# Kernel tuning notes

Hardware: AMD Instinct MI355X
Metric: run time of the kernel (lower is better)

## Reference

```python
import jax, jax.numpy as jnp
import numpy as np

D_MODEL = 512
N_HEADS = 8
D_KEYS = D_MODEL // N_HEADS  # 64
DIN = D_MODEL * 2            # 1024
DPROJ = D_KEYS * N_HEADS * 2 # 1024
B, L = 2, 2048


def setup_inputs() -> dict:
    key = jax.random.key(0)
    ks = jax.random.split(key, 11)
    s_in = 1.0 / np.sqrt(DIN)
    s_out = 1.0 / np.sqrt(DPROJ)
    return {
        "queries": jax.random.normal(ks[0], (B, L, DIN), jnp.float32),
        "keys": jax.random.normal(ks[1], (B, L, DIN), jnp.float32),
        "values": jax.random.normal(ks[2], (B, L, DIN), jnp.float32),
        "Wq": jax.random.normal(ks[3], (DPROJ, DIN), jnp.float32) * s_in,
        "bq": jax.random.normal(ks[4], (DPROJ,), jnp.float32) * s_in,
        "Wk": jax.random.normal(ks[5], (DPROJ, DIN), jnp.float32) * s_in,
        "bk": jax.random.normal(ks[6], (DPROJ,), jnp.float32) * s_in,
        "Wv": jax.random.normal(ks[7], (DPROJ, DIN), jnp.float32) * s_in,
        "bv": jax.random.normal(ks[8], (DPROJ,), jnp.float32) * s_in,
        "Wo": jax.random.normal(ks[9], (DIN, DPROJ), jnp.float32) * s_out,
        "bo": jax.random.normal(ks[10], (DIN,), jnp.float32) * s_out,
    }


def reference(queries, keys, values, Wq, bq, Wk, bk, Wv, bv, Wo, bo):
    b, l, _ = queries.shape
    H, E = N_HEADS, 2
    # projections: (B, L, DIN) -> (B, L, d_keys, H, 2)
    q = (queries @ Wq.T + bq).reshape(b, l, -1, H, E)
    k = (keys @ Wk.T + bk).reshape(b, l, -1, H, E)
    v = (values @ Wv.T + bv).reshape(b, l, -1, H, E)
    scale = 1.0 / np.sqrt(E)  # E=2 (real/imag)
    # attention over the d_keys axis, per token n, per head h
    scores = jnp.einsum('bnlhe,bnshe->bnhls', q, k)  # (B, L, H, dk, dk)
    A = jax.nn.softmax(scale * scores, axis=-1)
    out = jnp.einsum('bnhls,bnshd->bnlhd', A, v)     # (B, L, dk, H, 2)
    out = out.reshape(b, l, -1)                      # (B, L, dk*H*2)
    return out @ Wo.T + bo                           # (B, L, 2*d_model)
```

## Files before the change

### kernel.cpp

```cpp
#include <hip/hip_runtime.h>
#include <hip/hip_bf16.h>
#include <stdint.h>

#define TOK   4096
#define KDIM  1024
#define NDIM  1024
#define NHEAD 8

typedef _Float16 f16;
typedef __attribute__((ext_vector_type(8))) _Float16 f16x8;
typedef __attribute__((ext_vector_type(4))) float f32x4;

__device__ __forceinline__ void gload_lds16(const void* g, void* l) {
    __builtin_amdgcn_global_load_lds(
        (const __attribute__((address_space(1))) void*)g,
        (__attribute__((address_space(3))) void*)l, 16, 0, 0);
}

struct CvtArgs {
    const float* src[7];
    f16*         dst[7];
    int          n4[7];
};

__global__ __launch_bounds__(256) void cvt_kernel(CvtArgs a) {
    const int seg = blockIdx.y;
    const float4* s = (const float4*)a.src[seg];
    f16* d = a.dst[seg];
    const int n4 = a.n4[seg];
    const int stride = gridDim.x * blockDim.x;
    for (int i = blockIdx.x * blockDim.x + threadIdx.x; i < n4; i += stride) {
        float4 v = s[i];
        union { f16 h[4]; uint2 u; } o;
        o.h[0] = (f16)v.x; o.h[1] = (f16)v.y; o.h[2] = (f16)v.z; o.h[3] = (f16)v.w;
        *(uint2*)(d + (size_t)i * 4) = o.u;
    }
}

struct GemmArgs {
    const f16*   A[3];
    const f16*   B[3];
    const float* bias[3];
    void*        C[3];
};

#define VM_WAIT6 asm volatile("s_waitcnt vmcnt(6)" ::: "memory")
#define VM_WAIT0 asm volatile("s_waitcnt vmcnt(0)" ::: "memory")

template<int OUTMODE>
__global__ __launch_bounds__(256) void gemm_bt_kernel(GemmArgs ga) {
    constexpr int K = KDIM, N = NDIM;
    constexpr int NT = K / 64;
    const f16*   A    = ga.A[blockIdx.z];
    const f16*   B    = ga.B[blockIdx.z];
    const float* bias = ga.bias[blockIdx.z];

    __shared__ f16 sm[2 * (128 * 64 + 64 * 64)];

    const int tid  = threadIdx.x;
    const int wave = tid >> 6, lane = tid & 63;
    const int wm = wave >> 1, wn = wave & 1;
    const int bm = blockIdx.x * 128, bn = blockIdx.y * 64;
    const int lrow = lane & 15, kgrp = lane >> 4;

    f32x4 acc[4][2] = {};

    const int colL = (lane & 7) << 3;
    const int colG = (((lane & 7) ^ ((lane >> 3) & 7)) << 3);
    const int arow = wave * 32 + (lane >> 3);
    const int brow = wave * 16 + (lane >> 3);

    auto stage = [&](int buf, int kt) {
        f16* As = sm + buf * (128 * 64 + 64 * 64);
        f16* Bs = As + 128 * 64;
        #pragma unroll
        for (int i = 0; i < 4; ++i) {
            const int row = arow + i * 8;
            gload_lds16(A + (size_t)(bm + row) * K + kt + colG, As + row * 64 + colL);
        }
        #pragma unroll
        for (int i = 0; i < 2; ++i) {
            const int row = brow + i * 8;
            gload_lds16(B + (size_t)(bn + row) * K + kt + colG, Bs + row * 64 + colL);
        }
    };

    stage(0, 0);

    const int swz = (lrow & 7) << 3;

    for (int it = 0; it < NT; ++it) {
        const int cur = it & 1;
        if (it + 1 < NT) {
            stage(cur ^ 1, (it + 1) * 64);
            VM_WAIT6;
        } else {
            VM_WAIT0;
        }
        __builtin_amdgcn_s_barrier();
        __builtin_amdgcn_sched_barrier(0);

        const f16* As = sm + cur * (128 * 64 + 64 * 64);
        const f16* Bs = As + 128 * 64;
        #pragma unroll
        for (int kk = 0; kk < 2; ++kk) {
            f16x8 af[4], bf[2];
            const int kcol = (kk * 32 + kgrp * 8) ^ swz;
            #pragma unroll
            for (int mi = 0; mi < 4; ++mi)
                af[mi] = *(const f16x8*)(As + (wm * 64 + mi * 16 + lrow) * 64 + kcol);
            #pragma unroll
            for (int ni = 0; ni < 2; ++ni)
                bf[ni] = *(const f16x8*)(Bs + (wn * 32 + ni * 16 + lrow) * 64 + kcol);
            #pragma unroll
            for (int mi = 0; mi < 4; ++mi)
                #pragma unroll
                for (int ni = 0; ni < 2; ++ni)
                    acc[mi][ni] = __builtin_amdgcn_mfma_f32_16x16x32_f16(af[mi], bf[ni], acc[mi][ni], 0, 0, 0);
        }
        __builtin_amdgcn_s_barrier();
    }

    const int rbase = kgrp * 4;
    #pragma unroll
    for (int mi = 0; mi < 4; ++mi) {
        #pragma unroll
        for (int ni = 0; ni < 2; ++ni) {
            const int col = bn + wn * 32 + ni * 16 + lrow;
            const float bv = bias[col];
            #pragma unroll
            for (int r = 0; r < 4; ++r) {
                const int row = bm + wm * 64 + mi * 16 + rbase + r;
                const float v = acc[mi][ni][r] + bv;
                if constexpr (OUTMODE == 0)
                    ((f16*)ga.C[blockIdx.z])[(size_t)row * N + col] = (f16)v;
                else
                    ((float*)ga.C[blockIdx.z])[(size_t)row * N + col] = v;
            }
        }
    }
}

__global__ __launch_bounds__(512) void attn_kernel(const f16* qp, const f16* kp,
                                                   const f16* vp, f16* ao) {
    __shared__ uint qls[512], kls[512], vls[512], ols[512];
    const int tid = threadIdx.x, head = tid >> 6, lane = tid & 63;
    const int token = blockIdx.x;
    const size_t base = (size_t)token * 512;
    const float SCALE = 0.70710678118f * 1.44269504089f;

    qls[tid] = ((const uint*)qp)[base + tid];
    kls[tid] = ((const uint*)kp)[base + tid];
    vls[tid] = ((const uint*)vp)[base + tid];
    __syncthreads();

    union U2 { uint u; f16 h[2]; };
    U2 qu; qu.u = qls[lane * 8 + head];
    const float q0 = (float)qu.h[0] * SCALE, q1 = (float)qu.h[1] * SCALE;

    float sum = 0.f, o0 = 0.f, o1 = 0.f;
    #pragma unroll
    for (int s = 0; s < 64; ++s) {
        U2 ku, vu;
        ku.u = kls[s * 8 + head];
        vu.u = vls[s * 8 + head];
        const float p = exp2f(fmaf(q0, (float)ku.h[0], q1 * (float)ku.h[1]));
        sum += p;
        o0 = fmaf(p, (float)vu.h[0], o0);
        o1 = fmaf(p, (float)vu.h[1], o1);
    }
    const float inv = __builtin_amdgcn_rcpf(sum);
    U2 o;
    o.h[0] = (f16)(o0 * inv);
    o.h[1] = (f16)(o1 * inv);
    ols[lane * 8 + head] = o.u;
    __syncthreads();
    ((uint*)ao)[base + tid] = ols[tid];
}

extern "C" void kernel_launch(void* const* d_in, const int* in_sizes, int n_in,
                              void* d_out, int out_size, void* d_ws, size_t ws_size,
                              hipStream_t stream) {
    const float* queries = (const float*)d_in[0];
    const float* keys    = (const float*)d_in[1];
    const float* values  = (const float*)d_in[2];
    const float* Wq = (const float*)d_in[3];
    const float* bq = (const float*)d_in[4];
    const float* Wk = (const float*)d_in[5];
    const float* bk = (const float*)d_in[6];
    const float* Wv = (const float*)d_in[7];
    const float* bv = (const float*)d_in[8];
    const float* Wo = (const float*)d_in[9];
    const float* bo = (const float*)d_in[10];

    char* ws = (char*)d_ws;
    const size_t MB = 1024 * 1024;
    f16* Xq  = (f16*)(ws + 0 * MB);
    f16* Xk  = (f16*)(ws + 8 * MB);
    f16* Xv  = (f16*)(ws + 16 * MB);
    f16* Wqh = (f16*)(ws + 24 * MB);
    f16* Wkh = (f16*)(ws + 26 * MB);
    f16* Wvh = (f16*)(ws + 28 * MB);
    f16* Woh = (f16*)(ws + 30 * MB);
    f16* qp  = (f16*)(ws + 32 * MB);
    f16* kp  = (f16*)(ws + 40 * MB);
    f16* vp  = (f16*)(ws + 48 * MB);
    f16* ao  = (f16*)(ws + 56 * MB);

    CvtArgs ca;
    ca.src[0] = queries; ca.dst[0] = Xq;  ca.n4[0] = TOK * KDIM / 4;
    ca.src[1] = keys;    ca.dst[1] = Xk;  ca.n4[1] = TOK * KDIM / 4;
    ca.src[2] = values;  ca.dst[2] = Xv;  ca.n4[2] = TOK * KDIM / 4;
    ca.src[3] = Wq;      ca.dst[3] = Wqh; ca.n4[3] = NDIM * KDIM / 4;
    ca.src[4] = Wk;      ca.dst[4] = Wkh; ca.n4[4] = NDIM * KDIM / 4;
    ca.src[5] = Wv;      ca.dst[5] = Wvh; ca.n4[5] = NDIM * KDIM / 4;
    ca.src[6] = Wo;      ca.dst[6] = Woh; ca.n4[6] = NDIM * KDIM / 4;
    cvt_kernel<<<dim3(256, 7), 256, 0, stream>>>(ca);

    GemmArgs g1;
    g1.A[0] = Xq;  g1.A[1] = Xk;  g1.A[2] = Xv;
    g1.B[0] = Wqh; g1.B[1] = Wkh; g1.B[2] = Wvh;
    g1.bias[0] = bq; g1.bias[1] = bk; g1.bias[2] = bv;
    g1.C[0] = qp; g1.C[1] = kp; g1.C[2] = vp;
    gemm_bt_kernel<0><<<dim3(32, 16, 3), 256, 0, stream>>>(g1);

    attn_kernel<<<TOK, 512, 0, stream>>>(qp, kp, vp, ao);

    GemmArgs g2;
    g2.A[0] = ao; g2.B[0] = Woh; g2.bias[0] = bo; g2.C[0] = d_out;
    g2.A[1] = ao; g2.B[1] = Woh; g2.bias[1] = bo; g2.C[1] = d_out;
    g2.A[2] = ao; g2.B[2] = Woh; g2.bias[2] = bo; g2.C[2] = d_out;
    gemm_bt_kernel<1><<<dim3(32, 16, 1), 256, 0, stream>>>(g2);
}
```

Baseline: 210.1 us.

## Permute projection weight rows so attention reads head-contiguous data without LDS

```diff
diff --git a/kernel.cpp b/kernel.cpp
--- a/kernel.cpp
+++ b/kernel.cpp
@@ -8,8 +8,10 @@
 #define NHEAD 8
 
 typedef _Float16 f16;
+typedef __attribute__((ext_vector_type(2))) _Float16 h2;
 typedef __attribute__((ext_vector_type(8))) _Float16 f16x8;
 typedef __attribute__((ext_vector_type(4))) float f32x4;
+typedef __attribute__((ext_vector_type(4))) uint u32x4;
 
 __device__ __forceinline__ void gload_lds16(const void* g, void* l) {
     __builtin_amdgcn_global_load_lds(
@@ -17,23 +19,45 @@
         (__attribute__((address_space(3))) void*)l, 16, 0, 0);
 }
 
+
 struct CvtArgs {
     const float* src[7];
-    f16*         dst[7];
+    void*        dst[7];
     int          n4[7];
+    int          type[7];
 };
 
 __global__ __launch_bounds__(256) void cvt_kernel(CvtArgs a) {
     const int seg = blockIdx.y;
+    const int type = a.type[seg];
     const float4* s = (const float4*)a.src[seg];
-    f16* d = a.dst[seg];
     const int n4 = a.n4[seg];
     const int stride = gridDim.x * blockDim.x;
     for (int i = blockIdx.x * blockDim.x + threadIdx.x; i < n4; i += stride) {
         float4 v = s[i];
-        union { f16 h[4]; uint2 u; } o;
-        o.h[0] = (f16)v.x; o.h[1] = (f16)v.y; o.h[2] = (f16)v.z; o.h[3] = (f16)v.w;
-        *(uint2*)(d + (size_t)i * 4) = o.u;
+        if (type == 0) {
+            f16* d = (f16*)a.dst[seg];
+            union { f16 h[4]; uint2 u; } o;
+            o.h[0] = (f16)v.x; o.h[1] = (f16)v.y; o.h[2] = (f16)v.z; o.h[3] = (f16)v.w;
+            *(uint2*)(d + (size_t)i * 4) = o.u;
+        } else if (type == 1) {
+            f16* d = (f16*)a.dst[seg];
+            const int r = i >> 8, c = (i & 255) * 4;
+            const int rp = ((r >> 1) & 7) * 128 + (r >> 4) * 2 + (r & 1);
+            union { f16 h[4]; uint2 u; } o;
+            o.h[0] = (f16)v.x; o.h[1] = (f16)v.y; o.h[2] = (f16)v.z; o.h[3] = (f16)v.w;
+            *(uint2*)(d + (size_t)rp * 1024 + c) = o.u;
+        } else {
+            f16* d = (f16*)a.dst[seg];
+            const int r = i >> 8, c = (i & 255) * 4;
+            const int p0 = ((c >> 1) & 7) * 128 + (c >> 4) * 2;
+            const int p1 = (((c + 2) >> 1) & 7) * 128 + ((c + 2) >> 4) * 2;
+            union { f16 h[2]; uint u; } u01, u23;
+            u01.h[0] = (f16)v.x; u01.h[1] = (f16)v.y;
+            u23.h[0] = (f16)v.z; u23.h[1] = (f16)v.w;
+            *(uint*)(d + (size_t)r * 1024 + p0) = u01.u;
+            *(uint*)(d + (size_t)r * 1024 + p1) = u23.u;
+        }
     }
 }
 
@@ -127,7 +151,10 @@
         #pragma unroll
         for (int ni = 0; ni < 2; ++ni) {
             const int col = bn + wn * 32 + ni * 16 + lrow;
-            const float bv = bias[col];
+            const int bidx = (OUTMODE == 0)
+                ? (((col >> 1) & 63) * 16 + (col >> 7) * 2 + (col & 1))
+                : col;
+            const float bv = bias[bidx];
             #pragma unroll
             for (int r = 0; r < 4; ++r) {
                 const int row = bm + wm * 64 + mi * 16 + rbase + r;
@@ -141,41 +168,57 @@
     }
 }
 
-__global__ __launch_bounds__(512) void attn_kernel(const f16* qp, const f16* kp,
+__global__ __launch_bounds__(256) void attn_kernel(const f16* qp, const f16* kp,
                                                    const f16* vp, f16* ao) {
-    __shared__ uint qls[512], kls[512], vls[512], ols[512];
-    const int tid = threadIdx.x, head = tid >> 6, lane = tid & 63;
-    const int token = blockIdx.x;
-    const size_t base = (size_t)token * 512;
+    const int tid = threadIdx.x, wave = tid >> 6, lane = tid & 63;
+    const int task = blockIdx.x * 4 + wave;
+    const size_t base = (size_t)task * 64;
     const float SCALE = 0.70710678118f * 1.44269504089f;
 
-    qls[tid] = ((const uint*)qp)[base + tid];
-    kls[tid] = ((const uint*)kp)[base + tid];
-    vls[tid] = ((const uint*)vp)[base + tid];
-    __syncthreads();
-
-    union U2 { uint u; f16 h[2]; };
-    U2 qu; qu.u = qls[lane * 8 + head];
-    const float q0 = (float)qu.h[0] * SCALE, q1 = (float)qu.h[1] * SCALE;
+    union U2 { uint u; h2 h; f16 s[2]; };
+    U2 qu; qu.u = ((const uint*)qp)[base + lane];
+    const float q0 = (float)qu.s[0] * SCALE, q1 = (float)qu.s[1] * SCALE;
+#if __has_builtin(__builtin_amdgcn_fdot2)
+    h2 qs; qs[0] = (f16)q0; qs[1] = (f16)q1;
+#endif
+
+    const u32x4* kb = (const u32x4*)((const uint*)kp + base);
+    const u32x4* vb = (const u32x4*)((const uint*)vp + base);
 
     float sum = 0.f, o0 = 0.f, o1 = 0.f;
     #pragma unroll
-    for (int s = 0; s < 64; ++s) {
-        U2 ku, vu;
-        ku.u = kls[s * 8 + head];
-        vu.u = vls[s * 8 + head];
-        const float p = exp2f(fmaf(q0, (float)ku.h[0], q1 * (float)ku.h[1]));
-        sum += p;
-        o0 = fmaf(p, (float)vu.h[0], o0);
-        o1 = fmaf(p, (float)vu.h[1], o1);
+    for (int g = 0; g < 4; ++g) {
+        u32x4 kr[4], vr[4];
+        #pragma unroll
+        for (int i = 0; i < 4; ++i) { kr[i] = kb[g * 4 + i]; vr[i] = vb[g * 4 + i]; }
+        #pragma unroll
+        for (int i = 0; i < 4; ++i) {
+            #pragma unroll
+            for (int j = 0; j < 4; ++j) {
+                U2 ku, vu;
+                ku.u = kr[i][j];
+                vu.u = vr[i][j];
+#if __has_builtin(__builtin_amdgcn_fdot2)
+                const float sc = __builtin_amdgcn_fdot2(qs, ku.h, 0.0f, false);
+#else
+                const float sc = fmaf(q0, (float)ku.s[0], q1 * (float)ku.s[1]);
+#endif
+#if __has_builtin(__builtin_amdgcn_exp2f)
+                const float p = __builtin_amdgcn_exp2f(sc);
+#else
+                const float p = exp2f(sc);
+#endif
+                sum += p;
+                o0 = fmaf(p, (float)vu.s[0], o0);
+                o1 = fmaf(p, (float)vu.s[1], o1);
+            }
+        }
     }
     const float inv = __builtin_amdgcn_rcpf(sum);
     U2 o;
-    o.h[0] = (f16)(o0 * inv);
-    o.h[1] = (f16)(o1 * inv);
-    ols[lane * 8 + head] = o.u;
-    __syncthreads();
-    ((uint*)ao)[base + tid] = ols[tid];
+    o.s[0] = (f16)(o0 * inv);
+    o.s[1] = (f16)(o1 * inv);
+    ((uint*)ao)[base + lane] = o.u;
 }
 
 extern "C" void kernel_launch(void* const* d_in, const int* in_sizes, int n_in,
@@ -208,13 +251,13 @@
     f16* ao  = (f16*)(ws + 56 * MB);
 
     CvtArgs ca;
-    ca.src[0] = queries; ca.dst[0] = Xq;  ca.n4[0] = TOK * KDIM / 4;
-    ca.src[1] = keys;    ca.dst[1] = Xk;  ca.n4[1] = TOK * KDIM / 4;
-    ca.src[2] = values;  ca.dst[2] = Xv;  ca.n4[2] = TOK * KDIM / 4;
-    ca.src[3] = Wq;      ca.dst[3] = Wqh; ca.n4[3] = NDIM * KDIM / 4;
-    ca.src[4] = Wk;      ca.dst[4] = Wkh; ca.n4[4] = NDIM * KDIM / 4;
-    ca.src[5] = Wv;      ca.dst[5] = Wvh; ca.n4[5] = NDIM * KDIM / 4;
-    ca.src[6] = Wo;      ca.dst[6] = Woh; ca.n4[6] = NDIM * KDIM / 4;
+    ca.src[0] = queries; ca.dst[0] = Xq;  ca.n4[0] = TOK * KDIM / 4;  ca.type[0] = 0;
+    ca.src[1] = keys;    ca.dst[1] = Xk;  ca.n4[1] = TOK * KDIM / 4;  ca.type[1] = 0;
+    ca.src[2] = values;  ca.dst[2] = Xv;  ca.n4[2] = TOK * KDIM / 4;  ca.type[2] = 0;
+    ca.src[3] = Wq;      ca.dst[3] = Wqh; ca.n4[3] = NDIM * KDIM / 4; ca.type[3] = 1;
+    ca.src[4] = Wk;      ca.dst[4] = Wkh; ca.n4[4] = NDIM * KDIM / 4; ca.type[4] = 1;
+    ca.src[5] = Wv;      ca.dst[5] = Wvh; ca.n4[5] = NDIM * KDIM / 4; ca.type[5] = 1;
+    ca.src[6] = Wo;      ca.dst[6] = Woh; ca.n4[6] = NDIM * KDIM / 4; ca.type[6] = 2;
     cvt_kernel<<<dim3(256, 7), 256, 0, stream>>>(ca);
 
     GemmArgs g1;
@@ -224,7 +267,7 @@
     g1.C[0] = qp; g1.C[1] = kp; g1.C[2] = vp;
     gemm_bt_kernel<0><<<dim3(32, 16, 3), 256, 0, stream>>>(g1);
 
-    attn_kernel<<<TOK, 512, 0, stream>>>(qp, kp, vp, ao);
+    attn_kernel<<<TOK * NHEAD / 4, 256, 0, stream>>>(qp, kp, vp, ao);
 
     GemmArgs g2;
     g2.A[0] = ao; g2.B[0] = Woh; g2.bias[0] = bo; g2.C[0] = d_out;
```

Result: faster. 193.9 us (-7.7%).
